# Performance work log

Measured on AMD Instinct MI355X. Metric: run time of the kernel, lower is better.

The kernel has to match this reference:

```python
import jax, jax.numpy as jnp
import numpy as np

# S4D (diagonal state space) layer, version=1, bidirectional.
# Faithful to the standard minimal S4D: ZOH-discretized diagonal kernel via
# Vandermonde, causal FFT convolution, D skip, GELU, then 1x1-conv GLU.


def _s4d(u, log_dt, C_re, C_im, log_A_real, A_imag, D_skip, W_glu, b_glu):
    # u: (B, L, H)
    B, L, Hd = u.shape
    dt = jnp.exp(log_dt)                                   # (H,)
    A = -jnp.exp(log_A_real) + 1j * A_imag                 # (H, N2) complex
    dtA = A * dt[:, None]                                  # (H, N2)
    C = (C_re + 1j * C_im) * (jnp.exp(dtA) - 1.0) / A      # (H, N2)
    V = jnp.exp(dtA[:, :, None] * jnp.arange(L))           # (H, N2, L) Vandermonde
    K = 2.0 * jnp.einsum('hn,hnl->hl', C, V).real          # (H, L) SSM kernel
    uT = jnp.swapaxes(u, 1, 2)                             # (B, H, L)
    n = 2 * L                                              # zero-pad for causal conv
    y = jnp.fft.irfft(jnp.fft.rfft(uT, n=n) * jnp.fft.rfft(K, n=n), n=n)[..., :L]
    y = y + uT * D_skip[:, None]                           # skip connection
    y = jax.nn.gelu(y, approximate=False)                  # torch nn.GELU (exact erf)
    # output_linear: Conv1d(H, 2H, 1) + GLU(dim=-2)
    z = jnp.einsum('oh,bhl->bol', W_glu, y) + b_glu[None, :, None]
    y = z[:, :Hd] * jax.nn.sigmoid(z[:, Hd:])
    return jnp.swapaxes(y, 1, 2)                           # (B, L, H)


def setup_inputs() -> dict:
    key = jax.random.key(0)
    B, L, D, N = 64, 2048, 256, 64
    N2 = N // 2
    kx, kf, kr = jax.random.split(key, 3)

    def make_params(k0):
        ks = jax.random.split(k0, 6)
        log_dt = jax.random.uniform(ks[0], (D,)) * (np.log(0.1) - np.log(0.001)) + np.log(0.001)
        C_re = jax.random.normal(ks[1], (D, N2))
        C_im = jax.random.normal(ks[2], (D, N2))
        log_A_real = jnp.log(0.5 * jnp.ones((D, N2), dtype=jnp.float32))
        A_imag = np.pi * jnp.broadcast_to(jnp.arange(N2, dtype=jnp.float32), (D, N2))
        D_skip = jax.random.normal(ks[3], (D,))
        W_glu = jax.random.normal(ks[4], (2 * D, D)) / np.sqrt(D)
        b_glu = jax.random.normal(ks[5], (2 * D,)) * 0.01
        return log_dt, C_re, C_im, log_A_real, A_imag, D_skip, W_glu, b_glu

    pf = make_params(kf)
    pr = make_params(kr)
    names = ['log_dt', 'C_re', 'C_im', 'log_A_real', 'A_imag', 'D_skip', 'W_glu', 'b_glu']
    inp = {'x': jax.random.normal(kx, (B, L, D), dtype=jnp.float32)}
    for n_, v in zip(names, pf):
        inp[n_] = v
    for n_, v in zip(names, pr):
        inp[n_ + '_rev'] = v
    return inp


def reference(x, log_dt, C_re, C_im, log_A_real, A_imag, D_skip, W_glu, b_glu,
              log_dt_rev, C_re_rev, C_im_rev, log_A_real_rev, A_imag_rev,
              D_skip_rev, W_glu_rev, b_glu_rev):
    y_fwd = _s4d(x, log_dt, C_re, C_im, log_A_real, A_imag, D_skip, W_glu, b_glu)
    y_rev = _s4d(x[:, ::-1], log_dt_rev, C_re_rev, C_im_rev, log_A_real_rev,
                 A_imag_rev, D_skip_rev, W_glu_rev, b_glu_rev)
    return y_fwd + y_rev[:, ::-1]
```

## Files before the change

kernel.cpp:

```cpp
#include <hip/hip_runtime.h>
#include <hip/hip_bf16.h>
#include <math.h>

#define Bb 64
#define Ll 2048
#define Hh 256
#define N2v 32
#define NCH 4
#define CLEN (Ll / NCH)

#define WF_OFF 1024
#define BF_OFF 525312
#define GOLD_OFF 529408
#define A2_OFF 529408
#define AF_OFF 4723712
#define WT_OFF 13112320
#define XT_OFF 13243392
#define S_OFF  80352256
#define GT_OFF 214569984
#define WS_NEED 348787712ull
#define GNEW_OFF XT_OFF

typedef __hip_bfloat16 bf16;
typedef __bf16 bf16x8 __attribute__((ext_vector_type(8)));
typedef float f32x4 __attribute__((ext_vector_type(4)));
typedef _Float16 f16;
typedef _Float16 f16x2 __attribute__((ext_vector_type(2)));
typedef _Float16 f16x4 __attribute__((ext_vector_type(4)));
typedef _Float16 f16x8 __attribute__((ext_vector_type(8)));

__device__ __forceinline__ float b2f(bf16 v) { return __bfloat162float(v); }
__device__ __forceinline__ float ldf(const float* p, int i) { return p[i]; }
__device__ __forceinline__ float ldf(const bf16* p, int i) { return b2f(p[i]); }

__device__ __forceinline__ float4 ld4f(const float* p) { return *(const float4*)p; }
__device__ __forceinline__ float4 ld4f(const bf16* p) {
  ushort4 u = *(const ushort4*)p;
  float4 r;
  r.x = b2f(*(bf16*)&u.x); r.y = b2f(*(bf16*)&u.y);
  r.z = b2f(*(bf16*)&u.z); r.w = b2f(*(bf16*)&u.w);
  return r;
}

__device__ __forceinline__ void gl2lds16(const void* g, void* l) {
  __builtin_amdgcn_global_load_lds((const __attribute__((address_space(1))) void*)g,
                                   (__attribute__((address_space(3))) void*)l, 16, 0, 0);
}

__device__ __forceinline__ f32x4 mfma16(f16x8 a, f16x8 b, f32x4 c) {
  return __builtin_amdgcn_mfma_f32_16x16x32_f16(a, b, c, 0, 0, 0);
}

__device__ __forceinline__ bool input_is_bf16(const void* logA) {
  unsigned u = *(const unsigned*)logA;
  return (u >> 16) == (u & 0xffffu);
}

__global__ void s4d_prep(const void* Wf, const void* bfb, const void* Wr,
                         const void* brb, const void* logA, char* ws) {
  const bool bf = input_is_bf16(logA);
  bf16* wdst = (bf16*)(ws + WF_OFF);
  float* bdst = (float*)(ws + BF_OFF);
  const int i = blockIdx.x * 256 + threadIdx.x;
  if (i < 262144) {
    const int dstR = i >> 8, k = i & 255;
    const int ht = dstR >> 7, c = dstR & 127;
    const int mat = c >> 5, hl = c & 31;
    const int srow = mat * 256 + ht * 32 + hl;
    const void* src = (srow < 512) ? Wf : Wr;
    const int j = ((srow < 512) ? srow : srow - 512) * 256 + k;
    const float v = bf ? b2f(((const bf16*)src)[j]) : ((const float*)src)[j];
    wdst[i] = __float2bfloat16(v);
  } else if (i < 262144 + 1024) {
    const int j = i - 262144;
    const void* src = (j < 512) ? bfb : brb;
    const int k = (j < 512) ? j : j - 512;
    bdst[j] = bf ? b2f(((const bf16*)src)[k]) : ((const float*)src)[k];
  }
}

struct ScanP {
  const void* x;
  const void* prm[2][6];
  char* ws;
};

__global__ __launch_bounds__(64) void s4d_prepA(ScanP p) {
  const int d = blockIdx.x >> 8, h = blockIdx.x & 255;
  const int lane = threadIdx.x;
  __shared__ float Ksh[64];
  char* ws = p.ws;
  const bool bf = input_is_bf16(p.prm[0][3]);
#define LDP(w_, i_) (bf ? b2f(((const bf16*)p.prm[d][w_])[i_]) : ((const float*)p.prm[d][w_])[i_])
  const float dt = expf(LDP(0, h));
  const float dsk = LDP(5, h);
  float Kv = 0.f;
  const float dl = (float)lane;
  for (int n = 0; n < 32; ++n) {
    const int idx = h * 32 + n;
    const float Ar = -expf(LDP(3, idx));
    const float Ai = LDP(4, idx);
    const float th = Ai * dt, rr = Ar * dt;
    const float er = expf(rr);
    const float wr = er * cosf(th), wi = er * sinf(th);
    const float den = 1.f / (Ar * Ar + Ai * Ai);
    const float Er = wr - 1.f, Ei = wi;
    const float qr = (Er * Ar + Ei * Ai) * den, qi = (Ei * Ar - Er * Ai) * den;
    const float CR = LDP(1, idx), CI = LDP(2, idx);
    const float cre = 2.f * (CR * qr - CI * qi), cim = 2.f * (CR * qi + CI * qr);
    const float pe = expf(rr * dl), pang = th * dl;
    Kv += cre * pe * cosf(pang) - cim * pe * sinf(pang);
  }
  Ksh[lane] = Kv;
  if (lane < 32) {
    const int idx = h * 32 + lane;
    const float Ar = -expf(LDP(3, idx));
    const float Ai = LDP(4, idx);
    const float th = Ai * dt, rr = Ar * dt;
    const float e64 = expf(rr * 64.f);
    float2 wt;
    wt.x = e64 * cosf(th * 64.f);
    wt.y = e64 * sinf(th * 64.f);
    ((float2*)(ws + WT_OFF))[(d * 256 + h) * 32 + lane] = wt;
  }
  __syncthreads();
  f16* arow = (f16*)(ws + AF_OFF) + ((size_t)(d * 256 + h) * 64 + lane) * 128;
  for (int j = 0; j < 64; ++j) {
    float v = 0.f;
    if (d == 0) { if (j <= lane) v = Ksh[lane - j]; }
    else        { if (j >= lane) v = Ksh[j - lane]; }
    if (j == lane) v += dsk;
    arow[j] = (f16)v;
  }
  const float pexp = (d == 0) ? (float)(lane + 1) : (float)(64 - lane);
  for (int n = 0; n < 32; ++n) {
    const int idx = h * 32 + n;
    const float Ar = -expf(LDP(3, idx));
    const float Ai = LDP(4, idx);
    const float th = Ai * dt, rr = Ar * dt;
    const float er = expf(rr);
    const float wr = er * cosf(th), wi = er * sinf(th);
    const float den = 1.f / (Ar * Ar + Ai * Ai);
    const float Er = wr - 1.f, Ei = wi;
    const float qr = (Er * Ar + Ei * Ai) * den, qi = (Ei * Ar - Er * Ai) * den;
    const float CR = LDP(1, idx), CI = LDP(2, idx);
    const float cre = 2.f * (CR * qr - CI * qi), cim = 2.f * (CR * qi + CI * qr);
    const float pe = expf(rr * pexp), pang = th * pexp;
    const float pwr = pe * cosf(pang), pwi = pe * sinf(pang);
    arow[64 + 2 * n]     = (f16)(cre * pwr - cim * pwi);
    arow[64 + 2 * n + 1] = (f16)(-(cre * pwi + cim * pwr));
  }
  {
    const int n = lane >> 1, im = lane & 1;
    const int idx = h * 32 + n;
    const float Ar = -expf(LDP(3, idx));
    const float Ai = LDP(4, idx);
    const float th = Ai * dt, rr = Ar * dt;
    f16* a2 = (f16*)(ws + A2_OFF) + ((size_t)h * 128 + d * 64 + lane) * 64;
    for (int i = 0; i < 64; ++i) {
      const float pp = (d == 0) ? (float)(63 - i) : (float)i;
      const float e = expf(rr * pp), ang = th * pp;
      a2[i] = (f16)(im ? e * sinf(ang) : e * cosf(ang));
    }
  }
#undef LDP
}

template <typename T>
__device__ __forceinline__ void t1_body(const T* __restrict__ x, char* ws, float* tile) {
  const int b = blockIdx.x, h0 = blockIdx.y * 64;
  const int t = threadIdx.x;
  f16* xT = (f16*)(ws + XT_OFF);
  const int h4r = (t & 15) * 4;
  const int lrb = t >> 4;
  const int hw = t & 63;
  const int lo = t >> 6;
  const int lbase = blockIdx.z * 512;
  for (int l0 = lbase; l0 < lbase + 512; l0 += 64) {
    __syncthreads();
#pragma unroll
    for (int p = 0; p < 4; ++p) {
      const int l = p * 16 + lrb;
      const float4 v = ld4f(x + ((size_t)b * 2048 + l0 + l) * 256 + h0 + h4r);
      *(float4*)&tile[l * 68 + h4r] = v;
    }
    __syncthreads();
    f16x8 o0, o1;
#pragma unroll
    for (int j = 0; j < 8; ++j) o0[j] = (f16)tile[(lo * 16 + j) * 68 + hw];
#pragma unroll
    for (int j = 0; j < 8; ++j) o1[j] = (f16)tile[(lo * 16 + 8 + j) * 68 + hw];
    f16* dst = xT + ((size_t)(h0 + hw) * 64 + b) * 2048 + l0 + lo * 16;
    *(f16x8*)dst = o0;
    *(f16x8*)(dst + 8) = o1;
  }
}

__global__ __launch_bounds__(256) void s4d_t1(const void* x, const void* logA, char* ws) {
  __shared__ float tile[64 * 68];
  if (input_is_bf16(logA)) t1_body<bf16>((const bf16*)x, ws, tile);
  else                     t1_body<float>((const float*)x, ws, tile);
}

__global__ __launch_bounds__(256, 3) void s4d_krs(char* __restrict__ ws) {
  __shared__ char lds[34816];
  const int bid = blockIdx.x;
  const int h = ((bid >> 7) << 3) | (bid & 7);
  const int cb = (bid >> 3) & 15;
  const int t = threadIdx.x, lane = t & 63, wave = t >> 6;
  const int lm = lane & 15, lq = lane >> 4;
  const f16* xT = (const f16*)(ws + XT_OFF);
  const char* a2b = ws + A2_OFF + (size_t)h * 128 * 64 * 2;
  const int srow = lane >> 3;
  const int sch = (lane & 7) ^ srow;
#pragma unroll
  for (int j = 0; j < 4; ++j) {
    const int rb = wave * 4 + j;
    const int r = rb * 8 + srow;
    gl2lds16(a2b + r * 128 + sch * 16, lds + rb * 1024);
    const int col = cb * 128 + r;
    const int b_ = col >> 5, c_ = col & 31;
    gl2lds16((const char*)(xT + ((size_t)(h * 64 + b_) * 2048 + c_ * 64)) + sch * 16,
             lds + 16384 + rb * 1024);
  }
  __syncthreads();
  f32x4 acc[2][8];
#pragma unroll
  for (int i = 0; i < 2; ++i)
#pragma unroll
    for (int j = 0; j < 8; ++j) acc[i][j] = (f32x4){0.f, 0.f, 0.f, 0.f};
#pragma unroll
  for (int kb = 0; kb < 2; ++kb) {
    const int cA = kb * 4 + lq;
    f16x8 au[2], a2f[8];
#pragma unroll
    for (int i = 0; i < 2; ++i) {
      const int r = wave * 32 + i * 16 + lm;
      au[i] = *(const f16x8*)(lds + 16384 + r * 128 + ((cA ^ (r & 7)) * 16));
    }
#pragma unroll
    for (int j = 0; j < 8; ++j) {
      const int r = j * 16 + lm;
      a2f[j] = *(const f16x8*)(lds + r * 128 + ((cA ^ (r & 7)) * 16));
    }
#pragma unroll
    for (int i = 0; i < 2; ++i)
#pragma unroll
      for (int j = 0; j < 8; ++j) acc[i][j] = mfma16(au[i], a2f[j], acc[i][j]);
  }
  __syncthreads();
  f16* Cl = (f16*)lds;
#pragma unroll
  for (int i = 0; i < 2; ++i)
#pragma unroll
    for (int j = 0; j < 8; ++j)
#pragma unroll
      for (int r = 0; r < 4; ++r)
        Cl[(wave * 32 + i * 16 + lq * 4 + r) * 136 + j * 16 + lm] = (f16)acc[i][j][r];
  __syncthreads();
  const int n = t & 31, dir = (t >> 5) & 1, bl = wave;
  const float2 wt = ((const float2*)(ws + WT_OFF))[(dir * 256 + h) * 32 + n];
  f16* Sg = (f16*)(ws + S_OFF) + ((size_t)h * 2048 + cb * 128 + bl * 32) * 128 + dir * 64 + 2 * n;
  const f16* Cr = Cl + (size_t)(bl * 32) * 136 + dir * 64 + 2 * n;
  float sr = 0.f, si = 0.f;
  const int c0 = dir ? 31 : 0, cstep = dir ? -1 : 1;
  for (int it = 0; it < 32; ++it) {
    const int c = c0 + it * cstep;
    f16x2 sv; sv[0] = (f16)sr; sv[1] = (f16)si;
    *(f16x2*)(Sg + (size_t)c * 128) = sv;
    const float rr = (float)Cr[c * 136], ri = (float)Cr[c * 136 + 1];
    const float a = sr;
    sr = wt.x * a - wt.y * si + rr;
    si = wt.x * si + wt.y * a + ri;
  }
}

__global__ __launch_bounds__(256, 2) void s4d_k3(char* __restrict__ ws) {
  __shared__ char lds[57344];
  const int bid = blockIdx.x;
  const int h = ((bid >> 8) << 3) | (bid & 7);
  const int cb = (bid >> 3) & 31;
  const int t = threadIdx.x, lane = t & 63, wave = t >> 6;
  const int lm = lane & 15, lq = lane >> 4;
  const f16* xT = (const f16*)(ws + XT_OFF);
  const char* afb = ws + AF_OFF + (size_t)h * 64 * 128 * 2;
  const char* arb = ws + AF_OFF + (size_t)(256 + h) * 64 * 128 * 2;
  const char* sb = ws + S_OFF;
  {
    const int sr4 = lane >> 4, c16 = lane & 15;
#pragma unroll
    for (int j = 0; j < 4; ++j) {
      const int rb = wave * 4 + j;
      const int r = rb * 4 + sr4;
      const int sc = c16 ^ (r & 7);
      gl2lds16(afb + r * 256 + sc * 16, lds + rb * 1024);
      gl2lds16(arb + r * 256 + sc * 16, lds + 16384 + rb * 1024);
    }
  }
  {
    const int sr8 = lane >> 3, c8 = lane & 7;
#pragma unroll
    for (int j = 0; j < 2; ++j) {
      const int rb = wave * 2 + j;
      const int clr = rb * 8 + sr8;
      const int col = cb * 64 + clr;
      const int b_ = col >> 5, c_ = col & 31;
      const int sc = c8 ^ (clr & 7);
      gl2lds16((const char*)(xT + ((size_t)(h * 64 + b_) * 2048 + c_ * 64)) + sc * 16,
               lds + 32768 + rb * 1024);
      const char* srow = sb + ((size_t)h * 2048 + col) * 256;
      gl2lds16(srow + sc * 16,       lds + 40960 + rb * 1024);
      gl2lds16(srow + 128 + sc * 16, lds + 49152 + rb * 1024);
    }
  }
  __syncthreads();
  const int dir = wave >> 1, chf = wave & 1;
  const char* At = lds + dir * 16384;
  f32x4 acc[4][2];
#pragma unroll
  for (int i = 0; i < 4; ++i)
#pragma unroll
    for (int j = 0; j < 2; ++j) acc[i][j] = (f32x4){0.f, 0.f, 0.f, 0.f};
#pragma unroll
  for (int kb = 0; kb < 4; ++kb) {
    f16x8 av[4], bv[2];
    const int cA = kb * 4 + lq;
#pragma unroll
    for (int i = 0; i < 4; ++i) {
      const int r = i * 16 + lm;
      av[i] = *(const f16x8*)(At + r * 256 + ((cA ^ (r & 7)) * 16));
    }
    const char* Bt = lds + 32768 + ((kb < 2) ? 0 : (dir ? 16384 : 8192));
    const int cB = (kb & 1) * 4 + lq;
#pragma unroll
    for (int j = 0; j < 2; ++j) {
      const int r = chf * 32 + j * 16 + lm;
      bv[j] = *(const f16x8*)(Bt + r * 128 + ((cB ^ (r & 7)) * 16));
    }
#pragma unroll
    for (int i = 0; i < 4; ++i)
#pragma unroll
      for (int j = 0; j < 2; ++j) acc[i][j] = mfma16(av[i], bv[j], acc[i][j]);
  }
  f16* gT = (f16*)(ws + GT_OFF);
#pragma unroll
  for (int i = 0; i < 4; ++i)
#pragma unroll
    for (int j = 0; j < 2; ++j) {
      const int col = cb * 64 + chf * 32 + j * 16 + lm;
      const int b_ = col >> 5, c_ = col & 31;
      const int i0 = i * 16 + lq * 4;
      f16x4 o;
#pragma unroll
      for (int r = 0; r < 4; ++r) {
        const float y = acc[i][j][r];
        o[r] = (f16)(0.5f * y * (1.f + erff(y * 0.70710678118654752f)));
      }
      *(f16x4*)(gT + ((size_t)((dir * 256 + h) * 64 + b_)) * 2048 + c_ * 64 + i0) = o;
    }
}

__global__ __launch_bounds__(256) void s4d_tr(char* __restrict__ ws) {
  const int bid = blockIdx.x;
  const int mt = bid & 7, hq = (bid >> 3) & 7, b = (bid >> 6) & 63, dir = bid >> 12;
  const int lane = threadIdx.x & 63, wave = threadIdx.x >> 6;
  const int hb = hq * 32 + wave * 8;
  const f16* gT = (const f16*)(ws + GT_OFF);
  bf16* gm = (bf16*)(ws + GNEW_OFF) + (size_t)dir * (Bb * Ll * Hh);
#pragma unroll
  for (int mp = 0; mp < 4; ++mp) {
    const size_t l = (size_t)mt * 256 + mp * 64 + lane;
    ushort us[8];
#pragma unroll
    for (int e = 0; e < 8; ++e) {
      const float f = (float)gT[((size_t)((dir * 256 + hb + e) * 64 + b)) * 2048 + l];
      bf16 bb = __float2bfloat16(f);
      us[e] = *(ushort*)&bb;
    }
    uint4 o;
    o.x = (unsigned)us[0] | ((unsigned)us[1] << 16);
    o.y = (unsigned)us[2] | ((unsigned)us[3] << 16);
    o.z = (unsigned)us[4] | ((unsigned)us[5] << 16);
    o.w = (unsigned)us[6] | ((unsigned)us[7] << 16);
    *(uint4*)((char*)gm + ((size_t)b * 2048 + l) * 512 + hb * 2) = o;
  }
}

template <typename T>
__device__ __forceinline__ void scan_body(
    const T* __restrict__ x, const T* ldt_p, const T* cre_p, const T* cim_p,
    const T* lar_p, const T* aim_p, const T* dsk_p, bf16* gbase, float2* S) {
  const int t = threadIdx.x;
  const int lane = t & 63;
  const int ch = t >> 6;
  const int hloc = lane & 7;
  const int ngrp = lane >> 3;
  const int b = blockIdx.x;
  const int hblk = blockIdx.y;
  const int dir = blockIdx.z;
  const int h = hblk * 8 + hloc;

  const float dt = expf(ldf(ldt_p, h));
  float wre[4], wim[4], cre[4], cim[4], sre[4], sim[4];
#pragma unroll
  for (int j = 0; j < 4; ++j) {
    const int idx = h * N2v + ngrp * 4 + j;
    const float Ar = -expf(ldf(lar_p, idx));
    const float Ai = ldf(aim_p, idx);
    const float er = expf(Ar * dt);
    const float wr = er * cosf(Ai * dt), wi = er * sinf(Ai * dt);
    wre[j] = wr; wim[j] = wi;
    const float Er = wr - 1.0f, Ei = wi;
    const float den = 1.0f / (Ar * Ar + Ai * Ai);
    const float qr = (Er * Ar + Ei * Ai) * den;
    const float qi = (Ei * Ar - Er * Ai) * den;
    const float CR = ldf(cre_p, idx);
    const float CI = ldf(cim_p, idx);
    cre[j] = 2.0f * (CR * qr - CI * qi);
    cim[j] = 2.0f * (CR * qi + CI * qr);
    sre[j] = 0.0f; sim[j] = 0.0f;
  }
  const float dsk = ldf(dsk_p, h);

  const int base = b * (Ll * Hh) + h;
  const int stride = dir ? -Hh : Hh;
  const T* x0 = x + base + (dir ? (Ll - 1) * Hh : 0);
  bf16* g0 = gbase + dir * (Bb * Ll * Hh) + base + (dir ? (Ll - 1) * Hh : 0);

  if (ch < NCH - 1) {
    const T* xp = x0 + ch * CLEN * stride;
    for (int it = 0; it < CLEN / 4; ++it) {
      const float u0 = ldf(xp, 0);
      const float u1 = ldf(xp, stride);
      const float u2 = ldf(xp, 2 * stride);
      const float u3 = ldf(xp, 3 * stride);
      xp += 4 * stride;
#pragma unroll
      for (int k = 0; k < 4; ++k) {
        const float U = (k == 0) ? u0 : (k == 1) ? u1 : (k == 2) ? u2 : u3;
#pragma unroll
        for (int j = 0; j < 4; ++j) {
          const float a = sre[j], bb = sim[j];
          sre[j] = fmaf(wre[j], a, fmaf(-wim[j], bb, U));
          sim[j] = fmaf(wre[j], bb, wim[j] * a);
        }
      }
    }
#pragma unroll
    for (int j = 0; j < 4; ++j)
      S[((ch * 8 + ngrp) * 4 + j) * 8 + hloc] = (float2){sre[j], sim[j]};
  }
  __syncthreads();

  float pr[4], pi[4];
#pragma unroll
  for (int j = 0; j < 4; ++j) { pr[j] = wre[j]; pi[j] = wim[j]; }
  for (int q = 0; q < 9; ++q) {
#pragma unroll
    for (int j = 0; j < 4; ++j) {
      const float a = pr[j], bb = pi[j];
      pr[j] = fmaf(a, a, -bb * bb);
      pi[j] = 2.0f * a * bb;
    }
  }
#pragma unroll
  for (int j = 0; j < 4; ++j) { sre[j] = 0.0f; sim[j] = 0.0f; }
  for (int cc = 0; cc < ch; ++cc) {
#pragma unroll
    for (int j = 0; j < 4; ++j) {
      const float2 sv = S[((cc * 8 + ngrp) * 4 + j) * 8 + hloc];
      const float a = sre[j], bb = sim[j];
      sre[j] = fmaf(pr[j], a, fmaf(-pi[j], bb, sv.x));
      sim[j] = fmaf(pr[j], bb, fmaf(pi[j], a, sv.y));
    }
  }

  const T* xp = x0 + ch * CLEN * stride;
  bf16* gp = g0 + ch * CLEN * stride;
  const bool q0 = (ngrp & 1) != 0;
  const bool q1 = (ngrp & 2) != 0;
  const bool q2 = (ngrp & 4) != 0;
  for (int it = 0; it < CLEN / 8; ++it) {
    float u[8], P[8];
#pragma unroll
    for (int k = 0; k < 8; ++k) u[k] = ldf(xp, k * stride);
    xp += 8 * stride;
#pragma unroll
    for (int k = 0; k < 8; ++k) {
      float pa = 0.0f, pb = 0.0f;
#pragma unroll
      for (int j = 0; j < 4; ++j) {
        const float a = sre[j], bb = sim[j];
        sre[j] = fmaf(wre[j], a, fmaf(-wim[j], bb, u[k]));
        sim[j] = fmaf(wre[j], bb, wim[j] * a);
        pa = fmaf(cre[j], sre[j], pa);
        pb = fmaf(cim[j], sim[j], pb);
      }
      P[k] = pa - pb;
    }
    const float Q0 = (q0 ? P[1] : P[0]) + __shfl_xor(q0 ? P[0] : P[1], 8);
    const float Q1 = (q0 ? P[3] : P[2]) + __shfl_xor(q0 ? P[2] : P[3], 8);
    const float Q2 = (q0 ? P[5] : P[4]) + __shfl_xor(q0 ? P[4] : P[5], 8);
    const float Q3 = (q0 ? P[7] : P[6]) + __shfl_xor(q0 ? P[6] : P[7], 8);
    const float R0 = (q1 ? Q1 : Q0) + __shfl_xor(q1 ? Q0 : Q1, 16);
    const float R1 = (q1 ? Q3 : Q2) + __shfl_xor(q1 ? Q2 : Q3, 16);
    const float Tt = (q2 ? R1 : R0) + __shfl_xor(q2 ? R0 : R1, 32);
    const float s01 = q0 ? u[1] : u[0];
    const float s23 = q0 ? u[3] : u[2];
    const float s45 = q0 ? u[5] : u[4];
    const float s67 = q0 ? u[7] : u[6];
    const float Uo = q2 ? (q1 ? s67 : s45) : (q1 ? s23 : s01);
    const float y = fmaf(dsk, Uo, Tt);
    const float ge = 0.5f * y * (1.0f + erff(y * 0.70710678118654752f));
    gp[ngrp * stride] = __float2bfloat16(ge);
    gp += 8 * stride;
  }
}

__global__ __launch_bounds__(256) void s4d_scan(ScanP p) {
  __shared__ float2 S[(NCH - 1) * 8 * 4 * 8];
  const int dir = blockIdx.z;
  bf16* g = (bf16*)(p.ws + GOLD_OFF);
  if (input_is_bf16(p.prm[0][3])) {
    scan_body<bf16>((const bf16*)p.x, (const bf16*)p.prm[dir][0],
                    (const bf16*)p.prm[dir][1], (const bf16*)p.prm[dir][2],
                    (const bf16*)p.prm[dir][3], (const bf16*)p.prm[dir][4],
                    (const bf16*)p.prm[dir][5], g, S);
  } else {
    scan_body<float>((const float*)p.x, (const float*)p.prm[dir][0],
                     (const float*)p.prm[dir][1], (const float*)p.prm[dir][2],
                     (const float*)p.prm[dir][3], (const float*)p.prm[dir][4],
                     (const float*)p.prm[dir][5], g, S);
  }
}

__global__ __launch_bounds__(256, 3) void s4d_glu_gemm(const char* __restrict__ ws,
                                                       void* __restrict__ out_v,
                                                       const void* logA,
                                                       unsigned goff) {
  __shared__ char lds[49152];
  const bool obf = input_is_bf16(logA);
  const char* gf = ws + goff;
  const char* gr = gf + (size_t)Bb * Ll * Hh * 2;
  const char* wre = ws + WF_OFF;
  const float* bias = (const float*)(ws + BF_OFF);

  const int lane = threadIdx.x & 63;
  const int wave = threadIdx.x >> 6;
  const int lm = lane & 15;
  const int lq = lane >> 4;
  const int bid = blockIdx.x;
  const int mt = ((bid >> 6) << 3) | (bid & 7);
  const int ht = (bid >> 3) & 7;
  const size_t mrow0 = (size_t)mt * 128;

  f32x4 acc[4][4];
#pragma unroll
  for (int i = 0; i < 4; ++i)
#pragma unroll
    for (int ct = 0; ct < 4; ++ct) acc[i][ct] = (f32x4){0.f, 0.f, 0.f, 0.f};

  const int srow = lane >> 3;
  const int sch = (lane & 7) ^ srow;

  for (int ks = 0; ks < 4; ++ks) {
    const int kb_byte = ks * 128;
    __syncthreads();
#pragma unroll
    for (int j = 0; j < 12; ++j) {
      const int s = wave * 12 + j;
      const int tile = s >> 4;
      const int rb = s & 15;
      const int r = rb * 8 + srow;
      const char* gsrc;
      if (tile == 0)      gsrc = gf + (mrow0 + r) * 512 + kb_byte + sch * 16;
      else if (tile == 1) gsrc = gr + (mrow0 + r) * 512 + kb_byte + sch * 16;
      else                gsrc = wre + (size_t)(ht * 128 + r) * 512 + kb_byte + sch * 16;
      gl2lds16(gsrc, lds + tile * 16384 + rb * 1024);
    }
    __syncthreads();
    const char* Ab = lds + ((wave >> 1) ? 16384 : 0);
    const char* Bt = lds + 32768;
#pragma unroll
    for (int kb = 0; kb < 2; ++kb) {
      bf16x8 af[4], bf_[4];
      const int c = kb * 4 + lq;
#pragma unroll
      for (int i = 0; i < 4; ++i) {
        const int r = (wave & 1) * 64 + i * 16 + lm;
        af[i] = *(const bf16x8*)(Ab + r * 128 + ((c ^ (r & 7)) * 16));
      }
#pragma unroll
      for (int ct = 0; ct < 4; ++ct) {
        const int r = (wave >> 1) * 64 + ct * 16 + lm;
        bf_[ct] = *(const bf16x8*)(Bt + r * 128 + ((c ^ (r & 7)) * 16));
      }
#pragma unroll
      for (int i = 0; i < 4; ++i)
#pragma unroll
        for (int ct = 0; ct < 4; ++ct)
          acc[i][ct] = __builtin_amdgcn_mfma_f32_16x16x32_bf16(af[i], bf_[ct], acc[i][ct], 0, 0, 0);
    }
  }

  __syncthreads();
  float* xb = (float*)lds;
  if (wave >= 2) {
#pragma unroll
    for (int ctl = 0; ctl < 2; ++ctl) {
      const float blo = bias[512 + ht * 32 + ctl * 16 + lm];
      const float bhi = bias[768 + ht * 32 + ctl * 16 + lm];
#pragma unroll
      for (int i = 0; i < 4; ++i)
#pragma unroll
        for (int r = 0; r < 4; ++r) {
          const float z3 = acc[i][ctl][r] + blo;
          const float z4 = acc[i][ctl + 2][r] + bhi;
          xb[(((wave & 1) * 2 + ctl) * 16 + i * 4 + r) * 64 + lane] =
              z3 * (1.0f / (1.0f + expf(-z4)));
        }
    }
  }
  __syncthreads();
  if (wave < 2) {
#pragma unroll
    for (int ctl = 0; ctl < 2; ++ctl) {
      const int hout = ht * 32 + ctl * 16 + lm;
      const float blo = bias[hout];
      const float bhi = bias[256 + hout];
#pragma unroll
      for (int i = 0; i < 4; ++i)
#pragma unroll
        for (int r = 0; r < 4; ++r) {
          const float z1 = acc[i][ctl][r] + blo;
          const float z2 = acc[i][ctl + 2][r] + bhi;
          const float v = z1 * (1.0f / (1.0f + expf(-z2))) +
                          xb[(((wave & 1) * 2 + ctl) * 16 + i * 4 + r) * 64 + lane];
          const size_t m = mrow0 + (wave & 1) * 64 + i * 16 + lq * 4 + r;
          if (obf) ((bf16*)out_v)[m * Hh + hout] = __float2bfloat16(v);
          else     ((float*)out_v)[m * Hh + hout] = v;
        }
    }
  }
}

extern "C" void kernel_launch(void* const* d_in, const int* in_sizes, int n_in,
                              void* d_out, int out_size, void* d_ws, size_t ws_size,
                              hipStream_t stream) {
  ScanP p;
  p.x = d_in[0];
  for (int d = 0; d < 2; ++d)
    for (int j = 0; j < 6; ++j) p.prm[d][j] = d_in[1 + d * 8 + j];
  p.ws = (char*)d_ws;

  hipLaunchKernelGGL(s4d_prep, dim3(1028), dim3(256), 0, stream,
                     d_in[7], d_in[8], d_in[15], d_in[16], d_in[4], (char*)d_ws);

  if (ws_size >= (size_t)WS_NEED) {
    hipLaunchKernelGGL(s4d_prepA, dim3(512), dim3(64), 0, stream, p);
    hipLaunchKernelGGL(s4d_t1, dim3(64, 4, 4), dim3(256), 0, stream,
                       d_in[0], d_in[4], (char*)d_ws);
    hipLaunchKernelGGL(s4d_krs, dim3(4096), dim3(256), 0, stream, (char*)d_ws);
    hipLaunchKernelGGL(s4d_k3, dim3(8192), dim3(256), 0, stream, (char*)d_ws);
    hipLaunchKernelGGL(s4d_tr, dim3(8192), dim3(256), 0, stream, (char*)d_ws);
    hipLaunchKernelGGL(s4d_glu_gemm, dim3(8192), dim3(256), 0, stream,
                       (const char*)d_ws, d_out, d_in[4], (unsigned)GNEW_OFF);
  } else {
    hipLaunchKernelGGL(s4d_scan, dim3(Bb, Hh / 8, 2), dim3(256), 0, stream, p);
    hipLaunchKernelGGL(s4d_glu_gemm, dim3(8192), dim3(256), 0, stream,
                       (const char*)d_ws, d_out, d_in[4], (unsigned)GOLD_OFF);
  }
}
```

Measured before the change: 931.8 us.

## Double-buffer GLU GEMM K-tiles with async global-to-LDS prefetch

Replaces the single-buffered four-step K loop in the output GLU GEMM with eight smaller K steps over two LDS buffers. The next slice is prefetched with direct global-to-LDS loads while MFMAs run on the current one, using explicit vmcnt waits and barriers, and the swizzle changes to match 64-byte rows. MFMA issue priority is also raised with setprio. The aim is to hide global load latency behind compute, at the cost of more barriers and fragile hand-written waitcnt ordering.

```diff
diff --git a/kernel.cpp b/kernel.cpp
--- a/kernel.cpp
+++ b/kernel.cpp
@@ -560,48 +560,67 @@
 #pragma unroll
     for (int ct = 0; ct < 4; ++ct) acc[i][ct] = (f32x4){0.f, 0.f, 0.f, 0.f};
 
-  const int srow = lane >> 3;
-  const int sch = (lane & 7) ^ srow;
-
-  for (int ks = 0; ks < 4; ++ks) {
-    const int kb_byte = ks * 128;
-    __syncthreads();
-#pragma unroll
-    for (int j = 0; j < 12; ++j) {
-      const int s = wave * 12 + j;
-      const int tile = s >> 4;
-      const int rb = s & 15;
-      const int r = rb * 8 + srow;
-      const char* gsrc;
-      if (tile == 0)      gsrc = gf + (mrow0 + r) * 512 + kb_byte + sch * 16;
-      else if (tile == 1) gsrc = gr + (mrow0 + r) * 512 + kb_byte + sch * 16;
-      else                gsrc = wre + (size_t)(ht * 128 + r) * 512 + kb_byte + sch * 16;
-      gl2lds16(gsrc, lds + tile * 16384 + rb * 1024);
-    }
-    __syncthreads();
-    const char* Ab = lds + ((wave >> 1) ? 16384 : 0);
-    const char* Bt = lds + 32768;
-#pragma unroll
-    for (int kb = 0; kb < 2; ++kb) {
-      bf16x8 af[4], bf_[4];
-      const int c = kb * 4 + lq;
-#pragma unroll
-      for (int i = 0; i < 4; ++i) {
-        const int r = (wave & 1) * 64 + i * 16 + lm;
-        af[i] = *(const bf16x8*)(Ab + r * 128 + ((c ^ (r & 7)) * 16));
-      }
-#pragma unroll
-      for (int ct = 0; ct < 4; ++ct) {
-        const int r = (wave >> 1) * 64 + ct * 16 + lm;
-        bf_[ct] = *(const bf16x8*)(Bt + r * 128 + ((c ^ (r & 7)) * 16));
-      }
-#pragma unroll
-      for (int i = 0; i < 4; ++i)
-#pragma unroll
-        for (int ct = 0; ct < 4; ++ct)
-          acc[i][ct] = __builtin_amdgcn_mfma_f32_16x16x32_bf16(af[i], bf_[ct], acc[i][ct], 0, 0, 0);
-    }
-  }
+  const int srow16 = lane >> 2;
+  const int chunk = (lane & 3) ^ ((srow16 & 3) ^ ((srow16 >> 2) & 3));
+
+#define STAGE_KS(BUFI, KS2)                                                        \
+  do {                                                                             \
+    _Pragma("unroll")                                                              \
+    for (int j_ = 0; j_ < 6; ++j_) {                                               \
+      const int s_ = wave * 6 + j_;                                                \
+      const int tile_ = s_ >> 3;                                                   \
+      const int rb_ = s_ & 7;                                                      \
+      const int row_ = rb_ * 16 + srow16;                                          \
+      const char* gsrc_;                                                           \
+      if (tile_ == 0)                                                              \
+        gsrc_ = gf + (mrow0 + row_) * 512 + (KS2) * 64 + chunk * 16;               \
+      else if (tile_ == 1)                                                         \
+        gsrc_ = gr + (mrow0 + row_) * 512 + (KS2) * 64 + chunk * 16;               \
+      else                                                                         \
+        gsrc_ = wre + (size_t)(ht * 128 + row_) * 512 + (KS2) * 64 + chunk * 16;   \
+      gl2lds16(gsrc_, lds + (BUFI) * 24576 + tile_ * 8192 + rb_ * 1024);           \
+    }                                                                              \
+  } while (0)
+
+  STAGE_KS(0, 0);
+#pragma unroll
+  for (int ks = 0; ks < 8; ++ks) {
+    const int buf = ks & 1;
+    if (ks < 7) {
+      STAGE_KS(buf ^ 1, ks + 1);
+      asm volatile("s_waitcnt vmcnt(6)" ::: "memory");
+    } else {
+      asm volatile("s_waitcnt vmcnt(0)" ::: "memory");
+    }
+    __builtin_amdgcn_s_barrier();
+    __builtin_amdgcn_sched_barrier(0);
+    const char* Ab = lds + buf * 24576 + ((wave >> 1) ? 8192 : 0);
+    const char* Bt = lds + buf * 24576 + 16384;
+    bf16x8 af[4], bf_[4];
+#pragma unroll
+    for (int i = 0; i < 4; ++i) {
+      const int r = (wave & 1) * 64 + i * 16 + lm;
+      const int sw = (r & 3) ^ ((r >> 2) & 3);
+      af[i] = *(const bf16x8*)(Ab + r * 64 + ((lq ^ sw) * 16));
+    }
+#pragma unroll
+    for (int ct = 0; ct < 4; ++ct) {
+      const int r = (wave >> 1) * 64 + ct * 16 + lm;
+      const int sw = (r & 3) ^ ((r >> 2) & 3);
+      bf_[ct] = *(const bf16x8*)(Bt + r * 64 + ((lq ^ sw) * 16));
+    }
+    __builtin_amdgcn_s_setprio(1);
+#pragma unroll
+    for (int i = 0; i < 4; ++i)
+#pragma unroll
+      for (int ct = 0; ct < 4; ++ct)
+        acc[i][ct] = __builtin_amdgcn_mfma_f32_16x16x32_bf16(af[i], bf_[ct], acc[i][ct], 0, 0, 0);
+    __builtin_amdgcn_s_setprio(0);
+    __builtin_amdgcn_sched_barrier(0);
+    __builtin_amdgcn_s_barrier();
+    __builtin_amdgcn_sched_barrier(0);
+  }
+#undef STAGE_KS
 
   __syncthreads();
   float* xb = (float*)lds;
```

Result: faster. 820.0 us (-12.0%).
